# Performance work log

Hardware: AMD Instinct MI355X
Metric: run time of the kernel (lower is better)

## Reference

```python
import jax, jax.numpy as jnp
import numpy as np

B, SRC_L, DST_L, D = 1024, 256, 256, 64

def setup_inputs() -> dict:
    key = jax.random.key(0)
    k1, k2, k3, k4, k5, k6 = jax.random.split(key, 6)
    src_ids = jax.random.randint(k1, (B, SRC_L), 0, 10000, dtype=jnp.int32)
    dst_ids = jax.random.randint(k2, (B, DST_L), 0, 10000, dtype=jnp.int32)
    s1 = 1.0  # fan_in of first Linear is 1
    s2 = 1.0 / np.sqrt(D)
    W1 = jax.random.normal(k3, (D, 1), jnp.float32) * s1
    b1 = jax.random.normal(k4, (D,), jnp.float32) * s1
    W2 = jax.random.normal(k5, (D, D), jnp.float32) * s2
    b2 = jax.random.normal(k6, (D,), jnp.float32) * s2
    return {"src_ids": src_ids, "dst_ids": dst_ids, "W1": W1, "b1": b1, "W2": W2, "b2": b2}


def _appearances(src_ids, dst_ids):
    # count(x in seq) == sum over seq of (x == seq_j); exactly matches unique+bincount lookup
    src_in_src = (src_ids[:, :, None] == src_ids[:, None, :]).sum(-1)  # [B, Ls]
    dst_in_dst = (dst_ids[:, :, None] == dst_ids[:, None, :]).sum(-1)  # [B, Ld]
    eq_sd = src_ids[:, :, None] == dst_ids[:, None, :]                 # [B, Ls, Ld]
    src_in_dst = eq_sd.sum(-1)   # [B, Ls]
    dst_in_src = eq_sd.sum(1)    # [B, Ld]
    app_src = jnp.stack([src_in_src, src_in_dst], axis=-1).astype(jnp.float32)  # [B, Ls, 2]
    app_dst = jnp.stack([dst_in_src, dst_in_dst], axis=-1).astype(jnp.float32)  # [B, Ld, 2]
    app_src = jnp.where((src_ids == 0)[:, :, None], 0.0, app_src)
    app_dst = jnp.where((dst_ids == 0)[:, :, None], 0.0, app_dst)
    return app_src, app_dst


def _mlp_sum(app, W1, b1, W2, b2):
    # Linear(1,D) -> ReLU -> Linear(D,D), then sum over the 2 co-occurrence channels
    h = jax.nn.relu(app[..., None] * W1[:, 0] + b1)      # [B, L, 2, D]
    out = jnp.einsum('blcd,ed->blce', h, W2) + b2         # [B, L, 2, D]
    return out.sum(axis=2)                                # [B, L, D]


def reference(src_ids, dst_ids, W1, b1, W2, b2):
    app_src, app_dst = _appearances(src_ids, dst_ids)
    src_feat = _mlp_sum(app_src, W1, b1, W2, b2)
    dst_feat = _mlp_sum(app_dst, W1, b1, W2, b2)
    return (src_feat, dst_feat)
```

## Files before the change

### kernel.cpp

```cpp
#include <hip/hip_runtime.h>

#define BATCH 1024
#define L 256
#define D 64
#define NIDS 10000
#define TABN 257

__global__ void build_table_kernel(const float* __restrict__ W1,
                                   const float* __restrict__ b1,
                                   const float* __restrict__ W2,
                                   const float* __restrict__ b2,
                                   float* __restrict__ tab) {
    const int a = blockIdx.x;
    const int e = threadIdx.x;
    const float af = (float)a;
    float acc = b2[e];
    #pragma unroll
    for (int d = 0; d < D; ++d) {
        float h = af * W1[d] + b1[d];
        h = h > 0.0f ? h : 0.0f;
        acc += h * W2[e * D + d];
    }
    tab[a * D + e] = acc;
}

__global__ __launch_bounds__(256) void cooc_kernel(
        const int* __restrict__ src_ids,
        const int* __restrict__ dst_ids,
        const float* __restrict__ tab,
        float* __restrict__ out) {
    __shared__ unsigned int hist[2][NIDS / 2];
    __shared__ int          ids[2 * L];
    __shared__ unsigned int cnts[2 * L];

    const int b   = blockIdx.x;
    const int tid = threadIdx.x;

    unsigned int* h = &hist[0][0];
    #pragma unroll
    for (int i = tid; i < NIDS; i += 256) h[i] = 0u;

    const int sid = src_ids[b * L + tid];
    const int did = dst_ids[b * L + tid];
    ids[tid]     = sid;
    ids[L + tid] = did;
    __syncthreads();

    atomicAdd(&hist[0][sid >> 1], 1u << ((sid & 1) * 16));
    atomicAdd(&hist[1][did >> 1], 1u << ((did & 1) * 16));
    __syncthreads();

    {
        int id = ids[tid];
        unsigned c0 = (hist[0][id >> 1] >> ((id & 1) * 16)) & 0xffffu;
        unsigned c1 = (hist[1][id >> 1] >> ((id & 1) * 16)) & 0xffffu;
        if (id == 0) { c0 = 0u; c1 = 0u; }
        cnts[tid] = c0 | (c1 << 16);
        id = ids[L + tid];
        unsigned d0 = (hist[0][id >> 1] >> ((id & 1) * 16)) & 0xffffu;
        unsigned d1 = (hist[1][id >> 1] >> ((id & 1) * 16)) & 0xffffu;
        if (id == 0) { d0 = 0u; d1 = 0u; }
        cnts[L + tid] = d0 | (d1 << 16);
    }
    __syncthreads();

    const float4* tab4 = (const float4*)tab;
    float4*       out4 = (float4*)out;
    const int q  = tid & 15;
    const int pg = tid >> 4;
    const int ROW4 = D / 4;

    #pragma unroll 4
    for (int p = pg; p < 2 * L; p += 16) {
        const unsigned cp = cnts[p];
        const unsigned c1 = cp & 0xffffu;
        const unsigned c2 = cp >> 16;
        const float4 v1 = tab4[c1 * ROW4 + q];
        const float4 v2 = tab4[c2 * ROW4 + q];
        float4 v;
        v.x = v1.x + v2.x; v.y = v1.y + v2.y;
        v.z = v1.z + v2.z; v.w = v1.w + v2.w;
        int off;
        if (p < L) {
            off = b * (L * ROW4) + p * ROW4 + q;
        } else {
            off = BATCH * L * ROW4 + b * (L * ROW4) + (p - L) * ROW4 + q;
        }
        out4[off] = v;
    }
}

extern "C" void kernel_launch(void* const* d_in, const int* in_sizes, int n_in,
                              void* d_out, int out_size, void* d_ws, size_t ws_size,
                              hipStream_t stream) {
    const int*   src_ids = (const int*)d_in[0];
    const int*   dst_ids = (const int*)d_in[1];
    const float* W1      = (const float*)d_in[2];
    const float* b1      = (const float*)d_in[3];
    const float* W2      = (const float*)d_in[4];
    const float* b2      = (const float*)d_in[5];
    float*       out     = (float*)d_out;
    float*       tab     = (float*)d_ws;

    build_table_kernel<<<TABN, D, 0, stream>>>(W1, b1, W2, b2, tab);
    cooc_kernel<<<BATCH, 256, 0, stream>>>(src_ids, dst_ids, tab, out);
}
```

Measured before the change: 148.6 us.

## Halve LDS histogram to one reused buffer, use nontemporal output stores

The co-occurrence kernel now uses a single packed 16-bit histogram of about 20KB instead of two, building it first from src ids and then from dst ids with a re-zero in between. This halves LDS per block so more blocks can be resident per CU, at the cost of extra barriers and a second clear. Output writes are split into separate src and dst loops that use nontemporal stores to avoid polluting cache with the large write stream. The table-build kernel is repacked into 256-thread blocks and uses fma/fmax.

```diff
diff --git a/kernel.cpp b/kernel.cpp
--- a/kernel.cpp
+++ b/kernel.cpp
@@ -6,20 +6,25 @@
 #define NIDS 10000
 #define TABN 257
 
-__global__ void build_table_kernel(const float* __restrict__ W1,
-                                   const float* __restrict__ b1,
-                                   const float* __restrict__ W2,
-                                   const float* __restrict__ b2,
-                                   float* __restrict__ tab) {
-    const int a = blockIdx.x;
-    const int e = threadIdx.x;
+typedef float f32x4 __attribute__((ext_vector_type(4)));
+
+__global__ __launch_bounds__(256) void build_table_kernel(
+        const float* __restrict__ W1,
+        const float* __restrict__ b1,
+        const float* __restrict__ W2,
+        const float* __restrict__ b2,
+        float* __restrict__ tab) {
+    const int t = blockIdx.x * 256 + threadIdx.x;
+    const int a = t >> 6;
+    const int e = t & 63;
+    if (a >= TABN) return;
     const float af = (float)a;
     float acc = b2[e];
     #pragma unroll
     for (int d = 0; d < D; ++d) {
-        float h = af * W1[d] + b1[d];
-        h = h > 0.0f ? h : 0.0f;
-        acc += h * W2[e * D + d];
+        float h = fmaf(af, W1[d], b1[d]);
+        h = fmaxf(h, 0.0f);
+        acc = fmaf(h, W2[e * D + d], acc);
     }
     tab[a * D + e] = acc;
 }
@@ -29,64 +34,60 @@
         const int* __restrict__ dst_ids,
         const float* __restrict__ tab,
         float* __restrict__ out) {
-    __shared__ unsigned int hist[2][NIDS / 2];
-    __shared__ int          ids[2 * L];
+    __shared__ alignas(16) unsigned int hist[NIDS / 2];
     __shared__ unsigned int cnts[2 * L];
 
     const int b   = blockIdx.x;
     const int tid = threadIdx.x;
 
-    unsigned int* h = &hist[0][0];
-    #pragma unroll
-    for (int i = tid; i < NIDS; i += 256) h[i] = 0u;
-
     const int sid = src_ids[b * L + tid];
     const int did = dst_ids[b * L + tid];
-    ids[tid]     = sid;
-    ids[L + tid] = did;
+
+    uint4* h4 = (uint4*)hist;
+
+    for (int i = tid; i < NIDS / 8; i += 256) h4[i] = make_uint4(0u, 0u, 0u, 0u);
+    __syncthreads();
+    atomicAdd(&hist[sid >> 1], 1u << ((sid & 1) * 16));
+    __syncthreads();
+    unsigned c_ss = (hist[sid >> 1] >> ((sid & 1) * 16)) & 0xffffu;
+    unsigned c_ds = (hist[did >> 1] >> ((did & 1) * 16)) & 0xffffu;
     __syncthreads();
 
-    atomicAdd(&hist[0][sid >> 1], 1u << ((sid & 1) * 16));
-    atomicAdd(&hist[1][did >> 1], 1u << ((did & 1) * 16));
+    for (int i = tid; i < NIDS / 8; i += 256) h4[i] = make_uint4(0u, 0u, 0u, 0u);
+    __syncthreads();
+    atomicAdd(&hist[did >> 1], 1u << ((did & 1) * 16));
+    __syncthreads();
+    unsigned c_sd = (hist[sid >> 1] >> ((sid & 1) * 16)) & 0xffffu;
+    unsigned c_dd = (hist[did >> 1] >> ((did & 1) * 16)) & 0xffffu;
+
+    if (sid == 0) { c_ss = 0u; c_sd = 0u; }
+    if (did == 0) { c_ds = 0u; c_dd = 0u; }
+    cnts[tid]     = c_ss | (c_sd << 16);
+    cnts[L + tid] = c_ds | (c_dd << 16);
     __syncthreads();
 
-    {
-        int id = ids[tid];
-        unsigned c0 = (hist[0][id >> 1] >> ((id & 1) * 16)) & 0xffffu;
-        unsigned c1 = (hist[1][id >> 1] >> ((id & 1) * 16)) & 0xffffu;
-        if (id == 0) { c0 = 0u; c1 = 0u; }
-        cnts[tid] = c0 | (c1 << 16);
-        id = ids[L + tid];
-        unsigned d0 = (hist[0][id >> 1] >> ((id & 1) * 16)) & 0xffffu;
-        unsigned d1 = (hist[1][id >> 1] >> ((id & 1) * 16)) & 0xffffu;
-        if (id == 0) { d0 = 0u; d1 = 0u; }
-        cnts[L + tid] = d0 | (d1 << 16);
-    }
-    __syncthreads();
-
-    const float4* tab4 = (const float4*)tab;
-    float4*       out4 = (float4*)out;
-    const int q  = tid & 15;
-    const int pg = tid >> 4;
+    const f32x4* tab4 = (const f32x4*)tab;
+    f32x4*       out4 = (f32x4*)out;
+    const int q    = tid & 15;
+    const int pg   = tid >> 4;
     const int ROW4 = D / 4;
 
+    f32x4* osrc = out4 + (size_t)b * (L * ROW4);
+    f32x4* odst = out4 + (size_t)BATCH * L * ROW4 + (size_t)b * (L * ROW4);
+
     #pragma unroll 4
-    for (int p = pg; p < 2 * L; p += 16) {
+    for (int p = pg; p < L; p += 16) {
         const unsigned cp = cnts[p];
-        const unsigned c1 = cp & 0xffffu;
-        const unsigned c2 = cp >> 16;
-        const float4 v1 = tab4[c1 * ROW4 + q];
-        const float4 v2 = tab4[c2 * ROW4 + q];
-        float4 v;
-        v.x = v1.x + v2.x; v.y = v1.y + v2.y;
-        v.z = v1.z + v2.z; v.w = v1.w + v2.w;
-        int off;
-        if (p < L) {
-            off = b * (L * ROW4) + p * ROW4 + q;
-        } else {
-            off = BATCH * L * ROW4 + b * (L * ROW4) + (p - L) * ROW4 + q;
-        }
-        out4[off] = v;
+        const f32x4 v1 = tab4[(cp & 0xffffu) * ROW4 + q];
+        const f32x4 v2 = tab4[(cp >> 16) * ROW4 + q];
+        __builtin_nontemporal_store(v1 + v2, &osrc[p * ROW4 + q]);
+    }
+    #pragma unroll 4
+    for (int p = pg; p < L; p += 16) {
+        const unsigned cp = cnts[L + p];
+        const f32x4 v1 = tab4[(cp & 0xffffu) * ROW4 + q];
+        const f32x4 v2 = tab4[(cp >> 16) * ROW4 + q];
+        __builtin_nontemporal_store(v1 + v2, &odst[p * ROW4 + q]);
     }
 }
 
@@ -102,6 +103,6 @@
     float*       out     = (float*)d_out;
     float*       tab     = (float*)d_ws;
 
-    build_table_kernel<<<TABN, D, 0, stream>>>(W1, b1, W2, b2, tab);
+    build_table_kernel<<<(TABN * 64 + 255) / 256, 256, 0, stream>>>(W1, b1, W2, b2, tab);
     cooc_kernel<<<BATCH, 256, 0, stream>>>(src_ids, dst_ids, tab, out);
 }
```

Measured after the change: 153.8 us. 3.6% more time.
